# Optimization experiments

Hardware: AMD Instinct MI355X
Metric: run time of the kernel (lower is better)

The kernel has to match this reference:

```python
import jax, jax.numpy as jnp
import numpy as np

BN_EPS = 1e-5
NEG_SLOPE = 0.2  # PyG GATConv default negative_slope

N, E, D, H1, H2, OUT = 20000, 320000, 256, 256, 1024, 10


def setup_inputs() -> dict:
    key = jax.random.key(0)
    ks = jax.random.split(key, 16)
    rn = lambda k, s, sc=0.05: jax.random.normal(k, s, jnp.float32) * sc
    return {
        "x": rn(ks[0], (N, D), 1.0),
        "edge_index": jax.random.randint(ks[1], (2, E), 0, N, dtype=jnp.int64),
        "gc1_Ws": rn(ks[2], (D, H1)), "gc1_Wd": rn(ks[3], (D, H1)),
        "gc1_as": rn(ks[4], (H1,)), "gc1_ad": rn(ks[5], (H1,)), "gc1_b": jnp.zeros((H1,)),
        "gc2_Ws": rn(ks[6], (H1, H2)), "gc2_Wd": rn(ks[7], (H1, H2)),
        "gc2_as": rn(ks[8], (H2,)), "gc2_ad": rn(ks[9], (H2,)), "gc2_b": jnp.zeros((H2,)),
        "fc1_W": rn(ks[10], (H2, 4092)), "fc1_b": jnp.zeros((4092,)),
        "bn1_g": jnp.ones((4092,)), "bn1_b": jnp.zeros((4092,)),
        "fc2_W": rn(ks[11], (4092, 1024)), "fc2_b": jnp.zeros((1024,)),
        "bn2_g": jnp.ones((1024,)), "bn2_b": jnp.zeros((1024,)),
        "fc3_W": rn(ks[12], (1024, 256)), "fc3_b": jnp.zeros((256,)),
        "bn3_g": jnp.ones((256,)), "bn3_b": jnp.zeros((256,)),
        "fc4_W": rn(ks[13], (256, OUT)), "fc4_b": jnp.zeros((OUT,)),
    }


def gat_conv(x, src, dst, Ws, Wd, a_s, a_d, b):
    """PyG GATConv, heads=1: lin -> per-node attn logits -> gather ->
    LeakyReLU -> segment softmax over dst -> scatter-add, + bias."""
    n = x.shape[0]
    xs = x @ Ws                     # [N, F] source transform
    xd = x @ Wd                     # [N, F] target transform
    al_s = xs @ a_s                 # [N]
    al_d = xd @ a_d                 # [N]
    e = jax.nn.leaky_relu(al_s[src] + al_d[dst], NEG_SLOPE)   # [E]
    m = jax.ops.segment_max(e, dst, num_segments=n)
    ee = jnp.exp(e - m[dst])
    ssum = jax.ops.segment_sum(ee, dst, num_segments=n)
    alpha = ee / (ssum[dst] + 1e-16)                          # [E]
    out = jax.ops.segment_sum(alpha[:, None] * xs[src], dst, num_segments=n)
    return out + b


def batch_norm(x, g, b):
    mu = x.mean(0)
    var = ((x - mu) ** 2).mean(0)   # biased var, as torch BN training fwd
    return g * (x - mu) * jax.lax.rsqrt(var + BN_EPS) + b


def reference(x, edge_index,
              gc1_Ws, gc1_Wd, gc1_as, gc1_ad, gc1_b,
              gc2_Ws, gc2_Wd, gc2_as, gc2_ad, gc2_b,
              fc1_W, fc1_b, bn1_g, bn1_b,
              fc2_W, fc2_b, bn2_g, bn2_b,
              fc3_W, fc3_b, bn3_g, bn3_b,
              fc4_W, fc4_b):
    n = x.shape[0]
    # GATConv default add_self_loops=True
    loops = jnp.arange(n, dtype=edge_index.dtype)
    src = jnp.concatenate([edge_index[0], loops])
    dst = jnp.concatenate([edge_index[1], loops])

    h = jax.nn.relu(gat_conv(x, src, dst, gc1_Ws, gc1_Wd, gc1_as, gc1_ad, gc1_b))
    h = jax.nn.relu(gat_conv(h, src, dst, gc2_Ws, gc2_Wd, gc2_as, gc2_ad, gc2_b))
    h = jax.nn.relu(batch_norm(h @ fc1_W + fc1_b, bn1_g, bn1_b))
    h = jax.nn.relu(batch_norm(h @ fc2_W + fc2_b, bn2_g, bn2_b))
    h = jax.nn.relu(batch_norm(h @ fc3_W + fc3_b, bn3_g, bn3_b))
    h = h @ fc4_W + fc4_b
    return jax.nn.log_softmax(h, axis=-1)
```

## Files before the change

### kernel.cpp

```cpp
#include <hip/hip_runtime.h>

#define NN 20000
#define EE 320000
#define DD 256
#define HH1 256
#define HH2 1024
#define CC1 4092
#define CC1P 4096
#define OUTC 10
#define EA (EE + NN)

#define CEILDIV(a,b) (((a)+(b)-1)/(b))

typedef unsigned short u16;
typedef __attribute__((ext_vector_type(8))) short bf16x8;
typedef __attribute__((ext_vector_type(4))) float f32x4;

__device__ __forceinline__ float b2f(unsigned short u) {
  union { unsigned int i; float f; } v; v.i = ((unsigned int)u) << 16; return v.f;
}
__device__ __forceinline__ unsigned short f2b(float f) {
  unsigned int x = __float_as_uint(f);
  unsigned int r = (x + 0x7fffu + ((x >> 16) & 1u)) >> 16;
  return (unsigned short)r;
}

__device__ __forceinline__ void gload16(const u16* g, u16* l) {
  __builtin_amdgcn_global_load_lds(
      (const __attribute__((address_space(1))) unsigned int*)(unsigned long long)(const void*)g,
      (__attribute__((address_space(3))) unsigned int*)(unsigned int)(unsigned long long)(void*)l,
      16, 0, 0);
}

__global__ void k_zero32(unsigned int* __restrict__ p, int n) {
  int i = blockIdx.x * 256 + threadIdx.x;
  if (i < n) p[i] = 0u;
}

__global__ void k_f32_to_bf16(const float* __restrict__ in, u16* __restrict__ out, int n) {
  int i = blockIdx.x * 256 + threadIdx.x;
  if (i < n) out[i] = f2b(in[i]);
}

__global__ void k_convT(const float* __restrict__ in, u16* __restrict__ out,
                        int K, int N, int Kp) {
  __shared__ float tile[32][33];
  int kb = blockIdx.y * 32, nb = blockIdx.x * 32;
  int tx = threadIdx.x & 31, ty = threadIdx.x >> 5;
  #pragma unroll
  for (int i = 0; i < 32; i += 8) {
    int k = kb + ty + i, n = nb + tx;
    tile[ty + i][tx] = (k < K && n < N) ? in[(size_t)k * N + n] : 0.f;
  }
  __syncthreads();
  #pragma unroll
  for (int i = 0; i < 32; i += 8) {
    int n = nb + ty + i, k = kb + tx;
    if (n < N && k < Kp) out[(size_t)n * Kp + k] = f2b(tile[tx][ty + i]);
  }
}

__global__ void k_detect_e64(const int* __restrict__ ei, int* __restrict__ flag) {
  __shared__ int nz;
  if (threadIdx.x == 0) nz = 0;
  __syncthreads();
  if (ei[2 * threadIdx.x + 1] != 0) atomicOr(&nz, 1);
  __syncthreads();
  if (threadIdx.x == 0) *flag = (nz == 0) ? 1 : 0;
}

__device__ __forceinline__ int eread(const int* __restrict__ ei, int f64, int idx) {
  return f64 ? ei[(size_t)idx * 2] : ei[idx];
}

__global__ void k_proj_vec(const float* __restrict__ Ws, const float* __restrict__ as_,
                           const float* __restrict__ Wd, const float* __restrict__ ad_,
                           float* __restrict__ ps, float* __restrict__ pd, int K, int F) {
  int k = blockIdx.x;
  if (k >= K) return;
  int lane = threadIdx.x;
  const float* wsr = Ws + (size_t)k * F;
  const float* wdr = Wd + (size_t)k * F;
  float s = 0.f, d = 0.f;
  for (int f = lane * 4; f < F; f += 256) {
    float4 w1 = *(const float4*)(wsr + f);
    float4 a1 = *(const float4*)(as_ + f);
    float4 w2 = *(const float4*)(wdr + f);
    float4 a2 = *(const float4*)(ad_ + f);
    s += w1.x * a1.x + w1.y * a1.y + w1.z * a1.z + w1.w * a1.w;
    d += w2.x * a2.x + w2.y * a2.y + w2.z * a2.z + w2.w * a2.w;
  }
  #pragma unroll
  for (int off = 32; off > 0; off >>= 1) {
    s += __shfl_xor(s, off);
    d += __shfl_xor(d, off);
  }
  if (lane == 0) { ps[k] = s; pd[k] = d; }
}

__global__ void k_attn_logits(const u16* __restrict__ act, const float* __restrict__ ps,
                              const float* __restrict__ pd, float* __restrict__ als,
                              float* __restrict__ ald, int K) {
  int n = blockIdx.x;
  int lane = threadIdx.x;
  const u16* row = act + (size_t)n * K;
  float s = 0.f, d = 0.f;
  for (int k = lane; k < K; k += 64) {
    float v = b2f(row[k]);
    s += v * ps[k]; d += v * pd[k];
  }
  #pragma unroll
  for (int off = 32; off > 0; off >>= 1) { s += __shfl_down(s, off); d += __shfl_down(d, off); }
  if (lane == 0) { als[n] = s; ald[n] = d; }
}

__global__ void k_edge_count(const int* __restrict__ ei, const int* __restrict__ eflag,
                             int* __restrict__ counts) {
  int k = blockIdx.x * 256 + threadIdx.x;
  if (k >= EA) return;
  int f64 = *eflag;
  int dst = (k < EE) ? eread(ei, f64, EE + k) : (k - EE);
  if ((unsigned)dst < (unsigned)NN) atomicAdd(&counts[dst], 1);
}

__global__ void k_scan(const int* __restrict__ counts, int* __restrict__ rowptr,
                       int* __restrict__ cursor, int n) {
  __shared__ int sdata[1024];
  __shared__ int s_carry;
  if (threadIdx.x == 0) s_carry = 0;
  __syncthreads();
  for (int base = 0; base < n; base += 1024) {
    int idx = base + threadIdx.x;
    int v = (idx < n) ? counts[idx] : 0;
    sdata[threadIdx.x] = v;
    __syncthreads();
    for (int off = 1; off < 1024; off <<= 1) {
      int t = (threadIdx.x >= off) ? sdata[threadIdx.x - off] : 0;
      __syncthreads();
      sdata[threadIdx.x] += t;
      __syncthreads();
    }
    int incl = sdata[threadIdx.x];
    int carry = s_carry;
    if (idx < n) { int e = carry + incl - v; rowptr[idx] = e; cursor[idx] = e; }
    __syncthreads();
    if (threadIdx.x == 1023) s_carry = carry + sdata[1023];
    __syncthreads();
  }
  if (threadIdx.x == 0) rowptr[n] = s_carry;
}

__global__ void k_edge_fill(const int* __restrict__ ei, const int* __restrict__ eflag,
                            int* __restrict__ cursor, int* __restrict__ esrc) {
  int k = blockIdx.x * 256 + threadIdx.x;
  if (k >= EA) return;
  int f64 = *eflag;
  int src, dst;
  if (k < EE) { src = eread(ei, f64, k); dst = eread(ei, f64, EE + k); }
  else { src = dst = k - EE; }
  if ((unsigned)dst >= (unsigned)NN) return;
  if ((unsigned)src >= (unsigned)NN) src = 0;
  int pos = atomicAdd(&cursor[dst], 1);
  esrc[pos] = src;
}

#define ACHUNK 512
template<int FPT>
__global__ __launch_bounds__(256) void k_gat_aggregate(
    const int* __restrict__ rowptr, const int* __restrict__ esrc,
    const float* __restrict__ als, const float* __restrict__ ald,
    const u16* __restrict__ xs, const float* __restrict__ bias,
    u16* __restrict__ h, int F) {
  __shared__ float red[256];
  __shared__ float salpha[ACHUNK];
  __shared__ int   ssrc[ACHUNK];
  int n = blockIdx.x;
  int tid = threadIdx.x;
  int beg = rowptr[n], end = rowptr[n + 1];
  float ad = ald[n];

  float m = -1e30f;
  for (int j = beg + tid; j < end; j += 256) {
    float e = als[esrc[j]] + ad; e = (e < 0.f) ? 0.2f * e : e;
    m = fmaxf(m, e);
  }
  red[tid] = m; __syncthreads();
  #pragma unroll
  for (int s = 128; s > 0; s >>= 1) {
    if (tid < s) red[tid] = fmaxf(red[tid], red[tid + s]);
    __syncthreads();
  }
  m = red[0]; __syncthreads();

  float ss = 0.f;
  for (int j = beg + tid; j < end; j += 256) {
    float e = als[esrc[j]] + ad; e = (e < 0.f) ? 0.2f * e : e;
    ss += expf(e - m);
  }
  red[tid] = ss; __syncthreads();
  #pragma unroll
  for (int s = 128; s > 0; s >>= 1) {
    if (tid < s) red[tid] += red[tid + s];
    __syncthreads();
  }
  float inv = 1.f / (red[0] + 1e-16f); __syncthreads();

  float acc[FPT];
  #pragma unroll
  for (int i = 0; i < FPT; ++i) acc[i] = 0.f;
  int fbase = tid * FPT;
  for (int cbeg = beg; cbeg < end; cbeg += ACHUNK) {
    int cend = min(cbeg + ACHUNK, end);
    for (int j = cbeg + tid; j < cend; j += 256) {
      int s = esrc[j];
      float e = als[s] + ad; e = (e < 0.f) ? 0.2f * e : e;
      salpha[j - cbeg] = expf(e - m) * inv;
      ssrc[j - cbeg] = s;
    }
    __syncthreads();
    int cn = cend - cbeg;
    for (int j = 0; j < cn; ++j) {
      float a = salpha[j];
      const u16* rowp = xs + (size_t)ssrc[j] * F + fbase;
      if (FPT == 4) {
        ushort4 v4 = *(const ushort4*)rowp;
        acc[0] += a * b2f(v4.x);
        acc[1] += a * b2f(v4.y);
        acc[2] += a * b2f(v4.z);
        acc[3] += a * b2f(v4.w);
      } else {
        acc[0] += a * b2f(rowp[0]);
      }
    }
    __syncthreads();
  }
  #pragma unroll
  for (int i = 0; i < FPT; ++i) {
    int f = fbase + i;
    float v = acc[i] + bias[f];
    h[(size_t)n * F + f] = f2b(v > 0.f ? v : 0.f);
  }
}

template<bool BIAS, bool STATS>
__global__ __launch_bounds__(256, 2) void k_mfma_gemm(
    const u16* __restrict__ A, const u16* __restrict__ Bt,
    const float* __restrict__ bias, u16* __restrict__ C,
    int M, int N, int K, int ldc, int nbx,
    float* __restrict__ bsum, float* __restrict__ bsumsq) {
  __shared__ u16 lds[16384];
  int tid = threadIdx.x;
  int lane = tid & 63;
  int w = tid >> 6;

  int nwg = gridDim.x;
  int id = blockIdx.x;
  int q = nwg >> 3, r = nwg & 7;
  int xcd = id & 7, pos = id >> 3;
  int swz = (xcd < r ? xcd * (q + 1) : r * (q + 1) + (xcd - r) * q) + pos;
  int m0 = (swz / nbx) * 128, n0 = (swz % nbx) * 128;

  int dr = lane >> 2;
  int ss = (lane & 3) ^ ((lane >> 3) & 3);
  int lrow = lane & 15;
  int lk = lane >> 4;

  f32x4 acc[4][4] = {};
  int c0 = w * 4;

  auto STAGE = [&](int k0, int bufb) {
    #pragma unroll
    for (int j = 0; j < 4; ++j) {
      int c = c0 + j;
      int tr = ((c & 7) << 4) + dr;
      const u16* src;
      if (c < 8) {
        int rr = m0 + tr; rr = (rr < M) ? rr : (M - 1);
        src = A + (size_t)rr * K + k0 + ss * 8;
      } else {
        int rr = n0 + tr; rr = (rr < N) ? rr : (N - 1);
        src = Bt + (size_t)rr * K + k0 + ss * 8;
      }
      gload16(src, (u16*)((char*)lds + bufb + c * 1024));
    }
  };
  auto COMPUTE = [&](int bufb) {
    bf16x8 af[4], bfr[4];
    #pragma unroll
    for (int m = 0; m < 4; ++m) {
      int row = ((w >> 1) << 6) + m * 16 + lrow;
      af[m] = *(const bf16x8*)((const char*)lds + bufb + row * 64 +
                               ((lk ^ ((row >> 1) & 3)) << 4));
    }
    #pragma unroll
    for (int n = 0; n < 4; ++n) {
      int row = ((w & 1) << 6) + n * 16 + lrow;
      bfr[n] = *(const bf16x8*)((const char*)lds + bufb + 8192 + row * 64 +
                                ((lk ^ ((row >> 1) & 3)) << 4));
    }
    #pragma unroll
    for (int m = 0; m < 4; ++m)
      #pragma unroll
      for (int n = 0; n < 4; ++n)
        acc[m][n] = __builtin_amdgcn_mfma_f32_16x16x32_bf16(af[m], bfr[n], acc[m][n], 0, 0, 0);
  };

  int cur = 0;
  STAGE(0, 0);
  asm volatile("s_waitcnt vmcnt(0)" ::: "memory");
  __syncthreads();
  for (int k0 = 32; k0 < K; k0 += 32) {
    STAGE(k0, (cur ^ 1) * 16384);
    COMPUTE(cur * 16384);
    asm volatile("s_waitcnt vmcnt(0)" ::: "memory");
    __syncthreads();
    cur ^= 1;
  }
  COMPUTE(cur * 16384);

  int wrb = (w >> 1) * 64, wcb = (w & 1) * 64;
  float colS[4] = {0.f, 0.f, 0.f, 0.f}, colS2[4] = {0.f, 0.f, 0.f, 0.f};
  #pragma unroll
  for (int m = 0; m < 4; ++m) {
    #pragma unroll
    for (int qq = 0; qq < 4; ++qq) {
      int gm = m0 + wrb + m * 16 + lk * 4 + qq;
      bool okm = gm < M;
      #pragma unroll
      for (int n = 0; n < 4; ++n) {
        int gn = n0 + wcb + n * 16 + lrow;
        if (gn >= N) continue;
        float v = acc[m][n][qq];
        if (BIAS) v += bias[gn];
        if (okm) {
          C[(size_t)gm * ldc + gn] = f2b(v);
          if (STATS) { colS[n] += v; colS2[n] += v * v; }
        }
      }
    }
  }
  if (STATS) {
    #pragma unroll
    for (int n = 0; n < 4; ++n) {
      colS[n]  += __shfl_xor(colS[n], 16);
      colS[n]  += __shfl_xor(colS[n], 32);
      colS2[n] += __shfl_xor(colS2[n], 16);
      colS2[n] += __shfl_xor(colS2[n], 32);
    }
    if (lk == 0) {
      #pragma unroll
      for (int n = 0; n < 4; ++n) {
        int gn = n0 + wcb + n * 16 + lrow;
        if (gn < N) {
          atomicAdd(&bsum[gn], colS[n]);
          atomicAdd(&bsumsq[gn], colS2[n]);
        }
      }
    }
  }
}

__global__ void k_bn_finalize(const float* __restrict__ sum, const float* __restrict__ sumsq,
                              float* __restrict__ mu, float* __restrict__ rs, int C, float invN) {
  int c = blockIdx.x * 256 + threadIdx.x;
  if (c >= C) return;
  float m = sum[c] * invN;
  float var = fmaxf(sumsq[c] * invN - m * m, 0.f);
  mu[c] = m; rs[c] = rsqrtf(var + 1e-5f);
}

__global__ void k_bn_apply_relu(u16* __restrict__ h, const float* __restrict__ mu,
                                const float* __restrict__ rs, const float* __restrict__ g,
                                const float* __restrict__ b, long total4, int Ccols, int ld) {
  long i = (long)blockIdx.x * 256 + threadIdx.x;
  if (i >= total4) return;
  long e = i * 4;
  int c = (int)(e % Ccols);
  long r = e / Ccols;
  u16* p = h + (size_t)r * ld + c;
  ushort4 v = *(ushort4*)p;
  float f0 = b2f(v.x), f1 = b2f(v.y), f2 = b2f(v.z), f3 = b2f(v.w);
  f0 = g[c + 0] * (f0 - mu[c + 0]) * rs[c + 0] + b[c + 0];
  f1 = g[c + 1] * (f1 - mu[c + 1]) * rs[c + 1] + b[c + 1];
  f2 = g[c + 2] * (f2 - mu[c + 2]) * rs[c + 2] + b[c + 2];
  f3 = g[c + 3] * (f3 - mu[c + 3]) * rs[c + 3] + b[c + 3];
  v.x = f2b(f0 > 0.f ? f0 : 0.f);
  v.y = f2b(f1 > 0.f ? f1 : 0.f);
  v.z = f2b(f2 > 0.f ? f2 : 0.f);
  v.w = f2b(f3 > 0.f ? f3 : 0.f);
  *(ushort4*)p = v;
}

__global__ void k_fc4_logsoftmax(const u16* __restrict__ h, const float* __restrict__ W,
                                 const float* __restrict__ b, float* __restrict__ out) {
  int n = blockIdx.x;
  int lane = threadIdx.x;
  const u16* row = h + (size_t)n * HH1;
  float hv[4];
  #pragma unroll
  for (int j = 0; j < 4; ++j) hv[j] = b2f(row[lane + j * 64]);
  float logits[OUTC];
  #pragma unroll
  for (int o = 0; o < OUTC; ++o) {
    float p = 0.f;
    #pragma unroll
    for (int j = 0; j < 4; ++j) p += hv[j] * W[(size_t)(lane + j * 64) * OUTC + o];
    #pragma unroll
    for (int off = 32; off > 0; off >>= 1) p += __shfl_down(p, off);
    logits[o] = p;
  }
  if (lane == 0) {
    float mx = -1e30f;
    #pragma unroll
    for (int o = 0; o < OUTC; ++o) { logits[o] += b[o]; mx = fmaxf(mx, logits[o]); }
    float se = 0.f;
    #pragma unroll
    for (int o = 0; o < OUTC; ++o) se += expf(logits[o] - mx);
    float ls = mx + logf(se);
    #pragma unroll
    for (int o = 0; o < OUTC; ++o) out[(size_t)n * OUTC + o] = logits[o] - ls;
  }
}

extern "C" void kernel_launch(void* const* d_in, const int* in_sizes, int n_in,
                              void* d_out, int out_size, void* d_ws, size_t ws_size,
                              hipStream_t stream) {
  const float* x    = (const float*)d_in[0];
  const int*   ei   = (const int*)d_in[1];
  const float* g1Ws = (const float*)d_in[2];
  const float* g1Wd = (const float*)d_in[3];
  const float* g1as = (const float*)d_in[4];
  const float* g1ad = (const float*)d_in[5];
  const float* g1b  = (const float*)d_in[6];
  const float* g2Ws = (const float*)d_in[7];
  const float* g2Wd = (const float*)d_in[8];
  const float* g2as = (const float*)d_in[9];
  const float* g2ad = (const float*)d_in[10];
  const float* g2b  = (const float*)d_in[11];
  const float* f1W  = (const float*)d_in[12];
  const float* f1b  = (const float*)d_in[13];
  const float* bn1g = (const float*)d_in[14];
  const float* bn1b = (const float*)d_in[15];
  const float* f2W  = (const float*)d_in[16];
  const float* f2b_ = (const float*)d_in[17];
  const float* bn2g = (const float*)d_in[18];
  const float* bn2b = (const float*)d_in[19];
  const float* f3W  = (const float*)d_in[20];
  const float* f3b  = (const float*)d_in[21];
  const float* bn3g = (const float*)d_in[22];
  const float* bn3b = (const float*)d_in[23];
  const float* f4W  = (const float*)d_in[24];
  const float* f4b  = (const float*)d_in[25];
  float* out = (float*)d_out;
  (void)in_sizes; (void)n_in; (void)out_size; (void)ws_size;

  char* Wb = (char*)d_ws;
  size_t off = 0;
  auto alloc = [&](size_t bytes) -> char* {
    char* p = Wb + off;
    off = (off + bytes + 255) & ~(size_t)255;
    return p;
  };
  u16* h3   = (u16*)Wb;
  u16* xs2  = (u16*)alloc((size_t)NN * HH2 * 2);
  u16* xs1  = (u16*)alloc((size_t)NN * HH1 * 2);
  u16* xb   = (u16*)alloc((size_t)NN * DD * 2);
  u16* h1   = (u16*)alloc((size_t)NN * HH1 * 2);
  u16* h5   = (u16*)alloc((size_t)NN * HH1 * 2);
  u16* Bt1  = (u16*)alloc((size_t)HH1 * DD * 2);
  u16* Bt2  = (u16*)alloc((size_t)HH2 * HH1 * 2);
  int* esrc   = (int*)alloc((size_t)EA * 4);
  int* rowptr = (int*)alloc((NN + 1) * 4);
  int* cursor = (int*)alloc(NN * 4);
  int* counts = (int*)alloc(NN * 4);
  float* als1 = (float*)alloc(NN * 4);
  float* ald1 = (float*)alloc(NN * 4);
  float* als2 = (float*)alloc(NN * 4);
  float* ald2 = (float*)alloc(NN * 4);
  float* ps1  = (float*)alloc(1024 * 4);
  float* pd1  = (float*)alloc(1024 * 4);
  float* ps2  = (float*)alloc(1024 * 4);
  float* pd2  = (float*)alloc(1024 * 4);
  int* eflag  = (int*)alloc(256);

  off = ((size_t)NN * CC1P * 2 + 255) & ~(size_t)255;
  u16* h2 = (u16*)alloc((size_t)NN * HH2 * 2);
  u16* h4 = h2;
  u16* Bf = (u16*)alloc((size_t)HH2 * CC1P * 2);
  float* bsum   = (float*)alloc((size_t)CC1 * 2 * 4);
  float* bsumsq = bsum + CC1;
  float* bmu    = (float*)alloc((size_t)CC1 * 4);
  float* brs    = (float*)alloc((size_t)CC1 * 4);

  k_f32_to_bf16<<<CEILDIV(NN * DD, 256), 256, 0, stream>>>(x, xb, NN * DD);

  k_detect_e64<<<1, 256, 0, stream>>>(ei, eflag);
  k_zero32<<<CEILDIV(NN, 256), 256, 0, stream>>>((unsigned int*)counts, NN);
  k_edge_count<<<CEILDIV(EA, 256), 256, 0, stream>>>(ei, eflag, counts);
  k_scan<<<1, 1024, 0, stream>>>(counts, rowptr, cursor, NN);
  k_edge_fill<<<CEILDIV(EA, 256), 256, 0, stream>>>(ei, eflag, cursor, esrc);

  k_convT<<<dim3(CEILDIV(HH1, 32), CEILDIV(DD, 32)), 256, 0, stream>>>(g1Ws, Bt1, DD, HH1, DD);
  k_proj_vec<<<DD, 64, 0, stream>>>(g1Ws, g1as, g1Wd, g1ad, ps1, pd1, DD, HH1);
  k_attn_logits<<<NN, 64, 0, stream>>>(xb, ps1, pd1, als1, ald1, DD);
  k_mfma_gemm<false, false><<<CEILDIV(HH1, 128) * CEILDIV(NN, 128), 256, 0, stream>>>(
      xb, Bt1, nullptr, xs1, NN, HH1, DD, HH1, CEILDIV(HH1, 128), nullptr, nullptr);
  k_gat_aggregate<1><<<NN, 256, 0, stream>>>(rowptr, esrc, als1, ald1, xs1, g1b, h1, HH1);

  k_convT<<<dim3(CEILDIV(HH2, 32), CEILDIV(HH1, 32)), 256, 0, stream>>>(g2Ws, Bt2, HH1, HH2, HH1);
  k_proj_vec<<<HH1, 64, 0, stream>>>(g2Ws, g2as, g2Wd, g2ad, ps2, pd2, HH1, HH2);
  k_attn_logits<<<NN, 64, 0, stream>>>(h1, ps2, pd2, als2, ald2, HH1);
  k_mfma_gemm<false, false><<<CEILDIV(HH2, 128) * CEILDIV(NN, 128), 256, 0, stream>>>(
      h1, Bt2, nullptr, xs2, NN, HH2, HH1, HH2, CEILDIV(HH2, 128), nullptr, nullptr);
  k_gat_aggregate<4><<<NN, 256, 0, stream>>>(rowptr, esrc, als2, ald2, xs2, g2b, h2, HH2);

  k_convT<<<dim3(CEILDIV(CC1, 32), CEILDIV(HH2, 32)), 256, 0, stream>>>(f1W, Bf, HH2, CC1, HH2);
  k_zero32<<<CEILDIV(2 * CC1, 256), 256, 0, stream>>>((unsigned int*)bsum, 2 * CC1);
  k_mfma_gemm<true, true><<<CEILDIV(CC1, 128) * CEILDIV(NN, 128), 256, 0, stream>>>(
      h2, Bf, f1b, h3, NN, CC1, HH2, CC1P, CEILDIV(CC1, 128), bsum, bsumsq);
  k_bn_finalize<<<CEILDIV(CC1, 256), 256, 0, stream>>>(bsum, bsumsq, bmu, brs, CC1, 1.f / NN);
  k_bn_apply_relu<<<CEILDIV((long)NN * CC1 / 4, 256), 256, 0, stream>>>(
      h3, bmu, brs, bn1g, bn1b, (long)NN * CC1 / 4, CC1, CC1P);

  k_convT<<<dim3(CEILDIV(HH2, 32), CEILDIV(CC1P, 32)), 256, 0, stream>>>(f2W, Bf, CC1, HH2, CC1P);
  k_zero32<<<CEILDIV(2 * CC1, 256), 256, 0, stream>>>((unsigned int*)bsum, 2 * CC1);
  k_mfma_gemm<true, true><<<CEILDIV(HH2, 128) * CEILDIV(NN, 128), 256, 0, stream>>>(
      h3, Bf, f2b_, h4, NN, HH2, CC1P, HH2, CEILDIV(HH2, 128), bsum, bsumsq);
  k_bn_finalize<<<CEILDIV(HH2, 256), 256, 0, stream>>>(bsum, bsumsq, bmu, brs, HH2, 1.f / NN);
  k_bn_apply_relu<<<CEILDIV((long)NN * HH2 / 4, 256), 256, 0, stream>>>(
      h4, bmu, brs, bn2g, bn2b, (long)NN * HH2 / 4, HH2, HH2);

  k_convT<<<dim3(CEILDIV(HH1, 32), CEILDIV(HH2, 32)), 256, 0, stream>>>(f3W, Bf, HH2, HH1, HH2);
  k_zero32<<<CEILDIV(2 * CC1, 256), 256, 0, stream>>>((unsigned int*)bsum, 2 * CC1);
  k_mfma_gemm<true, true><<<CEILDIV(HH1, 128) * CEILDIV(NN, 128), 256, 0, stream>>>(
      h4, Bf, f3b, h5, NN, HH1, HH2, HH1, CEILDIV(HH1, 128), bsum, bsumsq);
  k_bn_finalize<<<CEILDIV(HH1, 256), 256, 0, stream>>>(bsum, bsumsq, bmu, brs, HH1, 1.f / NN);
  k_bn_apply_relu<<<CEILDIV((long)NN * HH1 / 4, 256), 256, 0, stream>>>(
      h5, bmu, brs, bn3g, bn3b, (long)NN * HH1 / 4, HH1, HH1);

  k_fc4_logsoftmax<<<NN, 64, 0, stream>>>(h5, f4W, f4b, out);
}
```

Before: 926.0 us.

## Overlap GEMM tile prefetch with compute and fold BN finalize into apply

```diff
diff --git a/kernel.cpp b/kernel.cpp
--- a/kernel.cpp
+++ b/kernel.cpp
@@ -305,18 +305,19 @@
         acc[m][n] = __builtin_amdgcn_mfma_f32_16x16x32_bf16(af[m], bfr[n], acc[m][n], 0, 0, 0);
   };
 
-  int cur = 0;
+  int nt = K >> 5;
   STAGE(0, 0);
-  asm volatile("s_waitcnt vmcnt(0)" ::: "memory");
-  __syncthreads();
-  for (int k0 = 32; k0 < K; k0 += 32) {
-    STAGE(k0, (cur ^ 1) * 16384);
-    COMPUTE(cur * 16384);
-    asm volatile("s_waitcnt vmcnt(0)" ::: "memory");
-    __syncthreads();
-    cur ^= 1;
-  }
-  COMPUTE(cur * 16384);
+  for (int t = 0; t < nt; ++t) {
+    if (t + 1 < nt) {
+      STAGE((t + 1) * 32, ((t + 1) & 1) * 16384);
+      asm volatile("s_waitcnt vmcnt(4)" ::: "memory");
+    } else {
+      asm volatile("s_waitcnt vmcnt(0)" ::: "memory");
+    }
+    __syncthreads();
+    COMPUTE((t & 1) * 16384);
+    __syncthreads();
+  }
 
   int wrb = (w >> 1) * 64, wcb = (w & 1) * 64;
   float colS[4] = {0.f, 0.f, 0.f, 0.f}, colS2[4] = {0.f, 0.f, 0.f, 0.f};
@@ -360,18 +361,10 @@
   }
 }
 
-__global__ void k_bn_finalize(const float* __restrict__ sum, const float* __restrict__ sumsq,
-                              float* __restrict__ mu, float* __restrict__ rs, int C, float invN) {
-  int c = blockIdx.x * 256 + threadIdx.x;
-  if (c >= C) return;
-  float m = sum[c] * invN;
-  float var = fmaxf(sumsq[c] * invN - m * m, 0.f);
-  mu[c] = m; rs[c] = rsqrtf(var + 1e-5f);
-}
-
-__global__ void k_bn_apply_relu(u16* __restrict__ h, const float* __restrict__ mu,
-                                const float* __restrict__ rs, const float* __restrict__ g,
-                                const float* __restrict__ b, long total4, int Ccols, int ld) {
+__global__ void k_bn_apply_relu(u16* __restrict__ h, const float* __restrict__ bsum,
+                                const float* __restrict__ bsumsq, const float* __restrict__ g,
+                                const float* __restrict__ b, long total4, int Ccols, int ld,
+                                float invN) {
   long i = (long)blockIdx.x * 256 + threadIdx.x;
   if (i >= total4) return;
   long e = i * 4;
@@ -379,15 +372,16 @@
   long r = e / Ccols;
   u16* p = h + (size_t)r * ld + c;
   ushort4 v = *(ushort4*)p;
-  float f0 = b2f(v.x), f1 = b2f(v.y), f2 = b2f(v.z), f3 = b2f(v.w);
-  f0 = g[c + 0] * (f0 - mu[c + 0]) * rs[c + 0] + b[c + 0];
-  f1 = g[c + 1] * (f1 - mu[c + 1]) * rs[c + 1] + b[c + 1];
-  f2 = g[c + 2] * (f2 - mu[c + 2]) * rs[c + 2] + b[c + 2];
-  f3 = g[c + 3] * (f3 - mu[c + 3]) * rs[c + 3] + b[c + 3];
-  v.x = f2b(f0 > 0.f ? f0 : 0.f);
-  v.y = f2b(f1 > 0.f ? f1 : 0.f);
-  v.z = f2b(f2 > 0.f ? f2 : 0.f);
-  v.w = f2b(f3 > 0.f ? f3 : 0.f);
+  float f[4] = { b2f(v.x), b2f(v.y), b2f(v.z), b2f(v.w) };
+  #pragma unroll
+  for (int j = 0; j < 4; ++j) {
+    float mu = bsum[c + j] * invN;
+    float var = fmaxf(bsumsq[c + j] * invN - mu * mu, 0.f);
+    float rs = rsqrtf(var + 1e-5f);
+    f[j] = g[c + j] * (f[j] - mu) * rs + b[c + j];
+    f[j] = f[j] > 0.f ? f[j] : 0.f;
+  }
+  v.x = f2b(f[0]); v.y = f2b(f[1]); v.z = f2b(f[2]); v.w = f2b(f[3]);
   *(ushort4*)p = v;
 }
 
@@ -491,6 +485,7 @@
   float* bsumsq = bsum + CC1;
   float* bmu    = (float*)alloc((size_t)CC1 * 4);
   float* brs    = (float*)alloc((size_t)CC1 * 4);
+  (void)bmu; (void)brs;
 
   k_f32_to_bf16<<<CEILDIV(NN * DD, 256), 256, 0, stream>>>(x, xb, NN * DD);
 
@@ -518,25 +513,22 @@
   k_zero32<<<CEILDIV(2 * CC1, 256), 256, 0, stream>>>((unsigned int*)bsum, 2 * CC1);
   k_mfma_gemm<true, true><<<CEILDIV(CC1, 128) * CEILDIV(NN, 128), 256, 0, stream>>>(
       h2, Bf, f1b, h3, NN, CC1, HH2, CC1P, CEILDIV(CC1, 128), bsum, bsumsq);
-  k_bn_finalize<<<CEILDIV(CC1, 256), 256, 0, stream>>>(bsum, bsumsq, bmu, brs, CC1, 1.f / NN);
   k_bn_apply_relu<<<CEILDIV((long)NN * CC1 / 4, 256), 256, 0, stream>>>(
-      h3, bmu, brs, bn1g, bn1b, (long)NN * CC1 / 4, CC1, CC1P);
+      h3, bsum, bsumsq, bn1g, bn1b, (long)NN * CC1 / 4, CC1, CC1P, 1.f / NN);
 
   k_convT<<<dim3(CEILDIV(HH2, 32), CEILDIV(CC1P, 32)), 256, 0, stream>>>(f2W, Bf, CC1, HH2, CC1P);
   k_zero32<<<CEILDIV(2 * CC1, 256), 256, 0, stream>>>((unsigned int*)bsum, 2 * CC1);
   k_mfma_gemm<true, true><<<CEILDIV(HH2, 128) * CEILDIV(NN, 128), 256, 0, stream>>>(
       h3, Bf, f2b_, h4, NN, HH2, CC1P, HH2, CEILDIV(HH2, 128), bsum, bsumsq);
-  k_bn_finalize<<<CEILDIV(HH2, 256), 256, 0, stream>>>(bsum, bsumsq, bmu, brs, HH2, 1.f / NN);
   k_bn_apply_relu<<<CEILDIV((long)NN * HH2 / 4, 256), 256, 0, stream>>>(
-      h4, bmu, brs, bn2g, bn2b, (long)NN * HH2 / 4, HH2, HH2);
+      h4, bsum, bsumsq, bn2g, bn2b, (long)NN * HH2 / 4, HH2, HH2, 1.f / NN);
 
   k_convT<<<dim3(CEILDIV(HH1, 32), CEILDIV(HH2, 32)), 256, 0, stream>>>(f3W, Bf, HH2, HH1, HH2);
   k_zero32<<<CEILDIV(2 * CC1, 256), 256, 0, stream>>>((unsigned int*)bsum, 2 * CC1);
   k_mfma_gemm<true, true><<<CEILDIV(HH1, 128) * CEILDIV(NN, 128), 256, 0, stream>>>(
       h4, Bf, f3b, h5, NN, HH1, HH2, HH1, CEILDIV(HH1, 128), bsum, bsumsq);
-  k_bn_finalize<<<CEILDIV(HH1, 256), 256, 0, stream>>>(bsum, bsumsq, bmu, brs, HH1, 1.f / NN);
   k_bn_apply_relu<<<CEILDIV((long)NN * HH1 / 4, 256), 256, 0, stream>>>(
-      h5, bmu, brs, bn3g, bn3b, (long)NN * HH1 / 4, HH1, HH1);
+      h5, bsum, bsumsq, bn3g, bn3b, (long)NN * HH1 / 4, HH1, HH1, 1.f / NN);
 
   k_fc4_logsoftmax<<<NN, 64, 0, stream>>>(h5, f4W, f4b, out);
 }
```

Result: slower. 959.1 us (+3.6%).
